# Kernel tuning notes

Hardware: AMD Instinct MI355X
Metric: run time of the kernel (lower is better)

Reference implementation:

```python
import jax, jax.numpy as jnp
import numpy as np

INPUT_DIM = 2048
OUTPUT_DIM = 16000
BATCH = 512


def _make_sketch(key, input_dim, output_dim):
    kh, ks = jax.random.split(key)
    rand_h = jax.random.randint(kh, (input_dim,), 0, output_dim)
    rand_s = (2 * jax.random.randint(ks, (input_dim,), 0, 2) - 1).astype(jnp.float32)
    # count-sketch matrix: one signed nonzero per row (duplicates sum, matching
    # torch.sparse .to_dense())
    return jnp.zeros((input_dim, output_dim), jnp.float32).at[jnp.arange(input_dim), rand_h].add(rand_s)


def setup_inputs() -> dict:
    key = jax.random.key(0)
    k1, k2, k3, k4 = jax.random.split(key, 4)
    return {
        "x1": jax.random.normal(k1, (BATCH, INPUT_DIM), jnp.float32),
        "x2": jax.random.normal(k2, (BATCH, INPUT_DIM), jnp.float32),
        "sketch1": _make_sketch(k3, INPUT_DIM, OUTPUT_DIM),
        "sketch2": _make_sketch(k4, INPUT_DIM, OUTPUT_DIM),
    }


def reference(x1, x2, sketch1, sketch2):
    d = sketch1.shape[1]  # output_dim
    # count-sketch projection (dense GEMM, as in the original)
    p1 = x1 @ sketch1  # [B, D]
    p2 = x2 @ sketch2  # [B, D]
    # circular convolution via FFT
    f1 = jnp.fft.rfft(p1, axis=-1)
    f2 = jnp.fft.rfft(p2, axis=-1)
    # torch.irfft (old API) did NOT normalize -> equals numpy irfft * D; the
    # module then multiplies by output_dim again, matching `* self.output_dim`.
    cbp = jnp.fft.irfft(f1 * f2, n=d, axis=-1) * d
    # signed square root
    ss = jnp.sqrt(jax.nn.relu(cbp)) - jnp.sqrt(jax.nn.relu(-cbp))
    # L2 normalize along dim=0 (the batch dim, as written in the original)
    norm = jnp.sqrt(jnp.sum(ss * ss, axis=0, keepdims=True))
    return ss / jnp.maximum(norm, 1e-12)
```

## Files before the change

### kernel.cpp

```cpp
#include <hip/hip_runtime.h>
#include <math.h>

#define D_OUT 16000
#define IN_DIM 2048
#define BATCH 512
#define T2 1024
#define PAD 129

typedef float floatx4 __attribute__((ext_vector_type(4)));

__device__ __forceinline__ float2 cmul(float2 a, float2 b) {
    return make_float2(a.x * b.x - a.y * b.y, a.x * b.y + a.y * b.x);
}
__device__ __forceinline__ float2 cadd(float2 a, float2 b) { return make_float2(a.x + b.x, a.y + b.y); }
__device__ __forceinline__ float2 csub(float2 a, float2 b) { return make_float2(a.x - b.x, a.y - b.y); }

__device__ __forceinline__ int PZ(int j, int i) { return j * PAD + i; }

template<int INV>
__device__ __forceinline__ float2 ctw(float2 w) { if (INV) w.y = -w.y; return w; }

__device__ __forceinline__ int div125(int m) { return (int)(((unsigned)m * 33555u) >> 22); }

template<int INV>
__device__ __forceinline__ float2 bigtw(int m, const float2* w128f, const float2* wNf) {
    int a = div125(m);
    int b = m - a * 125;
    float2 r = cmul(w128f[a], wNf[b]);
    if (INV) r.y = -r.y;
    return r;
}

template<int INV>
__device__ __forceinline__ void dft5(float2& b0, float2& b1, float2& b2, float2& b3, float2& b4) {
    const float C1 = 0.30901699437494742f, S1 = 0.95105651629515357f;
    const float C2 = -0.80901699437494745f, S2 = 0.58778525229247314f;
    float2 t1 = cadd(b1, b4), t2 = csub(b1, b4);
    float2 t3 = cadd(b2, b3), t4 = csub(b2, b3);
    float2 X0 = make_float2(b0.x + t1.x + t3.x, b0.y + t1.y + t3.y);
    float2 m1 = make_float2(b0.x + C1 * t1.x + C2 * t3.x, b0.y + C1 * t1.y + C2 * t3.y);
    float2 m2 = make_float2(b0.x + C2 * t1.x + C1 * t3.x, b0.y + C2 * t1.y + C1 * t3.y);
    float2 n1 = make_float2(S1 * t2.x + S2 * t4.x, S1 * t2.y + S2 * t4.y);
    float2 n2 = make_float2(S2 * t2.x - S1 * t4.x, S2 * t2.y - S1 * t4.y);
    if (!INV) {
        b1 = make_float2(m1.x + n1.y, m1.y - n1.x);
        b4 = make_float2(m1.x - n1.y, m1.y + n1.x);
        b2 = make_float2(m2.x + n2.y, m2.y - n2.x);
        b3 = make_float2(m2.x - n2.y, m2.y + n2.x);
    } else {
        b1 = make_float2(m1.x - n1.y, m1.y + n1.x);
        b4 = make_float2(m1.x + n1.y, m1.y - n1.x);
        b2 = make_float2(m2.x - n2.y, m2.y + n2.x);
        b3 = make_float2(m2.x + n2.y, m2.y - n2.x);
    }
    b0 = X0;
}

__global__ void extract_kernel(const float* __restrict__ sk1, const float* __restrict__ sk2,
                               int* __restrict__ h1, float* __restrict__ s1,
                               int* __restrict__ h2, float* __restrict__ s2) {
    int row = blockIdx.x & (IN_DIM - 1);
    bool second = blockIdx.x >= IN_DIM;
    const float* sk = second ? sk2 : sk1;
    const floatx4* base = (const floatx4*)(sk + (size_t)row * D_OUT);
    const int t = threadIdx.x;
    float hacc = 0.f, sacc = 0.f;
    floatx4 v[5];
#pragma unroll
    for (int batch = 0; batch < 3; batch++) {
#pragma unroll
        for (int c = 0; c < 5; c++)
            v[c] = __builtin_nontemporal_load(&base[t + 256 * (5 * batch + c)]);
#pragma unroll
        for (int c = 0; c < 5; c++) {
            float j4 = (float)(4 * (t + 256 * (5 * batch + c)));
            hacc += j4 * fabsf(v[c].x) + (j4 + 1.f) * fabsf(v[c].y) +
                    (j4 + 2.f) * fabsf(v[c].z) + (j4 + 3.f) * fabsf(v[c].w);
            sacc += v[c].x + v[c].y + v[c].z + v[c].w;
        }
    }
    if (t < 160) {
        floatx4 vt = __builtin_nontemporal_load(&base[3840 + t]);
        float j4 = (float)(4 * (3840 + t));
        hacc += j4 * fabsf(vt.x) + (j4 + 1.f) * fabsf(vt.y) +
                (j4 + 2.f) * fabsf(vt.z) + (j4 + 3.f) * fabsf(vt.w);
        sacc += vt.x + vt.y + vt.z + vt.w;
    }
#pragma unroll
    for (int off = 32; off; off >>= 1) {
        hacc += __shfl_down(hacc, off);
        sacc += __shfl_down(sacc, off);
    }
    __shared__ float sh[8];
    int lane = t & 63, wv = t >> 6;
    if (lane == 0) { sh[wv] = hacc; sh[wv + 4] = sacc; }
    __syncthreads();
    if (t == 0) {
        float h = sh[0] + sh[1] + sh[2] + sh[3];
        float s = sh[4] + sh[5] + sh[6] + sh[7];
        int* hh = second ? h2 : h1;
        float* ss = second ? s2 : s1;
        hh[row] = (int)(h + 0.5f);
        ss[row] = s;
    }
}

__global__ void __launch_bounds__(T2, 1) cbp_kernel(
    const float* __restrict__ x1, const float* __restrict__ x2,
    const int* __restrict__ h1, const float* __restrict__ s1,
    const int* __restrict__ h2, const float* __restrict__ s2,
    float* __restrict__ out) {
    __shared__ float2 smem[125 * PAD + 1 + 125 + 128 + 125];
    float2* z = smem;
    float2* w125 = smem + 125 * PAD + 1;
    float2* w128f = w125 + 125;
    float2* wNf = w128f + 128;
    const int tid = threadIdx.x;
    const int b = blockIdx.x;

    for (int t = tid; t < 125; t += T2) {
        float s, c;
        sincospif(t * (2.0f / 125.0f), &s, &c);
        w125[t] = make_float2(c, -s);
        sincospif(t * (1.0f / 8000.0f), &s, &c);
        wNf[t] = make_float2(c, -s);
    }
    for (int a = tid; a < 128; a += T2) {
        float s, c;
        sincospif(a * (1.0f / 64.0f), &s, &c);
        w128f[a] = make_float2(c, -s);
    }
    {
        float4* z4 = (float4*)z;
        for (int i = tid; i < 8063; i += T2) z4[i] = make_float4(0.f, 0.f, 0.f, 0.f);
    }
    __syncthreads();

    const float* x1r = x1 + (size_t)b * IN_DIM;
    const float* x2r = x2 + (size_t)b * IN_DIM;
    float* zf = (float*)z;
    for (int i = tid; i < IN_DIM; i += T2) {
        int n1 = h1[i] >> 7, n2 = h1[i] & 127;
        int jr = 25 * (n1 % 5) + 5 * ((n1 / 5) % 5) + n1 / 25;
        atomicAdd(&zf[2 * PZ(jr, n2)], x1r[i] * s1[i]);
        n1 = h2[i] >> 7; n2 = h2[i] & 127;
        jr = 25 * (n1 % 5) + 5 * ((n1 / 5) % 5) + n1 / 25;
        atomicAdd(&zf[2 * PZ(jr, n2) + 1], x2r[i] * s2[i]);
    }
    __syncthreads();

    for (int w = tid; w < 3200; w += T2) {
        int i = w & 127, g = w >> 7;
        int p = PZ(5 * g, i);
        float2 b0 = z[p], b1 = z[p + PAD], b2 = z[p + 2 * PAD], b3 = z[p + 3 * PAD], b4 = z[p + 4 * PAD];
        dft5<0>(b0, b1, b2, b3, b4);
        z[p] = b0; z[p + PAD] = b1; z[p + 2 * PAD] = b2; z[p + 3 * PAD] = b3; z[p + 4 * PAD] = b4;
    }
    __syncthreads();
    for (int w = tid; w < 3200; w += T2) {
        int i = w & 127, j5 = w >> 7;
        int g = j5 / 5, q = j5 - 5 * g;
        int p = PZ(g * 25 + q, i);
        float2 b0 = z[p];
        float2 b1 = cmul(z[p + 5 * PAD], w125[q * 5]);
        float2 b2 = cmul(z[p + 10 * PAD], w125[q * 10]);
        float2 b3 = cmul(z[p + 15 * PAD], w125[q * 15]);
        float2 b4 = cmul(z[p + 20 * PAD], w125[q * 20]);
        dft5<0>(b0, b1, b2, b3, b4);
        z[p] = b0; z[p + 5 * PAD] = b1; z[p + 10 * PAD] = b2; z[p + 15 * PAD] = b3; z[p + 20 * PAD] = b4;
    }
    __syncthreads();
    for (int w = tid; w < 3200; w += T2) {
        int i = w & 127, q = w >> 7;
        int p = PZ(q, i);
        float2 b0 = z[p];
        float2 b1 = cmul(z[p + 25 * PAD], w125[q]);
        float2 b2 = cmul(z[p + 50 * PAD], w125[q * 2]);
        float2 b3 = cmul(z[p + 75 * PAD], w125[q * 3]);
        float2 b4 = cmul(z[p + 100 * PAD], w125[q * 4]);
        dft5<0>(b0, b1, b2, b3, b4);
        z[p]             = cmul(b0, bigtw<0>(i * q, w128f, wNf));
        z[p + 25 * PAD]  = cmul(b1, bigtw<0>(i * (q + 25), w128f, wNf));
        z[p + 50 * PAD]  = cmul(b2, bigtw<0>(i * (q + 50), w128f, wNf));
        z[p + 75 * PAD]  = cmul(b3, bigtw<0>(i * (q + 75), w128f, wNf));
        z[p + 100 * PAD] = cmul(b4, bigtw<0>(i * (q + 100), w128f, wNf));
    }
    __syncthreads();

    if (tid < 1000) {
        int q = tid / 125, j = tid - q * 125;
        int p = PZ(j, q);
        float2 x[16];
#pragma unroll
        for (int t = 0; t < 16; t++) x[t] = z[p + 8 * t];
#pragma unroll
        for (int t = 0; t < 8; t++) {
            float2 u = cadd(x[t], x[t + 8]);
            float2 d = csub(x[t], x[t + 8]);
            x[t + 8] = cmul(d, w128f[q + 8 * t]);
            x[t] = u;
        }
#pragma unroll
        for (int h = 0; h < 16; h += 8)
            for (int t = h; t < h + 4; t++) {
                float2 u = cadd(x[t], x[t + 4]);
                float2 d = csub(x[t], x[t + 4]);
                x[t + 4] = cmul(d, w128f[2 * q + 16 * (t & 7)]);
                x[t] = u;
            }
#pragma unroll
        for (int h = 0; h < 16; h += 4)
            for (int t = h; t < h + 2; t++) {
                float2 u = cadd(x[t], x[t + 2]);
                float2 d = csub(x[t], x[t + 2]);
                x[t + 2] = cmul(d, w128f[4 * q + 32 * (t & 3)]);
                x[t] = u;
            }
        {
            float2 w16 = w128f[8 * q];
#pragma unroll
            for (int t = 0; t < 16; t += 2) {
                float2 u = cadd(x[t], x[t + 1]);
                float2 d = csub(x[t], x[t + 1]);
                x[t + 1] = cmul(d, w16);
                x[t] = u;
            }
        }
#pragma unroll
        for (int t = 0; t < 16; t++) z[p + 8 * t] = x[t];
    }
    __syncthreads();
    for (int idx = tid; idx < 2000; idx += T2) {
        int g = idx / 125, j = idx - g * 125;
        int p = PZ(j, 8 * g);
        float2 x[8];
#pragma unroll
        for (int d = 0; d < 8; d++) x[d] = z[p + d];
#pragma unroll
        for (int d = 0; d < 4; d++) {
            float2 u = cadd(x[d], x[d + 4]);
            float2 v = csub(x[d], x[d + 4]);
            x[d + 4] = cmul(v, w128f[16 * d]);
            x[d] = u;
        }
#pragma unroll
        for (int h = 0; h < 8; h += 4) {
            float2 u = cadd(x[h], x[h + 2]);
            float2 v = csub(x[h], x[h + 2]);
            x[h] = u; x[h + 2] = v;
            u = cadd(x[h + 1], x[h + 3]);
            v = csub(x[h + 1], x[h + 3]);
            x[h + 1] = u;
            x[h + 3] = make_float2(v.y, -v.x);
        }
#pragma unroll
        for (int d = 0; d < 8; d += 2) {
            float2 u = cadd(x[d], x[d + 1]);
            float2 v = csub(x[d], x[d + 1]);
            x[d] = u; x[d + 1] = v;
        }
#pragma unroll
        for (int d = 0; d < 8; d++) z[p + d] = x[d];
    }
    __syncthreads();

    for (int k = tid; k <= 8000; k += T2) {
        int k1 = k % 125, k2 = k / 125;
        int km = (k == 0) ? 0 : 16000 - k;
        int k1m = km % 125, k2m = km / 125;
        int p = PZ(k1, __brev((unsigned)k2) >> 25);
        int pm = PZ(k1m, __brev((unsigned)k2m) >> 25);
        float2 Zk = z[p], Zm = z[pm];
        float2 F1 = make_float2(0.5f * (Zk.x + Zm.x), 0.5f * (Zk.y - Zm.y));
        float2 F2 = make_float2(0.5f * (Zk.y + Zm.y), -0.5f * (Zk.x - Zm.x));
        float2 G = cmul(F1, F2);
        z[p] = G;
        z[pm] = make_float2(G.x, -G.y);
    }
    __syncthreads();

    for (int idx = tid; idx < 2000; idx += T2) {
        int g = idx / 125, j = idx - g * 125;
        int p = PZ(j, 8 * g);
        float2 x[8];
#pragma unroll
        for (int d = 0; d < 8; d++) x[d] = z[p + d];
#pragma unroll
        for (int d = 0; d < 8; d += 2) {
            float2 t = x[d + 1];
            x[d + 1] = csub(x[d], t);
            x[d] = cadd(x[d], t);
        }
#pragma unroll
        for (int h = 0; h < 8; h += 4) {
            float2 t = x[h + 2];
            x[h + 2] = csub(x[h], t);
            x[h] = cadd(x[h], t);
            float2 s = x[h + 3];
            t = make_float2(-s.y, s.x);
            x[h + 3] = csub(x[h + 1], t);
            x[h + 1] = cadd(x[h + 1], t);
        }
#pragma unroll
        for (int d = 0; d < 4; d++) {
            float2 t = cmul(ctw<1>(w128f[16 * d]), x[d + 4]);
            x[d + 4] = csub(x[d], t);
            x[d] = cadd(x[d], t);
        }
#pragma unroll
        for (int d = 0; d < 8; d++) z[p + d] = x[d];
    }
    __syncthreads();
    if (tid < 1000) {
        int q = tid / 125, j = tid - q * 125;
        int p = PZ(j, q);
        float2 x[16];
#pragma unroll
        for (int t = 0; t < 16; t++) x[t] = z[p + 8 * t];
        {
            float2 w16 = ctw<1>(w128f[8 * q]);
#pragma unroll
            for (int t = 0; t < 16; t += 2) {
                float2 tt = cmul(w16, x[t + 1]);
                x[t + 1] = csub(x[t], tt);
                x[t] = cadd(x[t], tt);
            }
        }
#pragma unroll
        for (int h = 0; h < 16; h += 4)
            for (int t = h; t < h + 2; t++) {
                float2 w = ctw<1>(w128f[4 * q + 32 * (t & 3)]);
                float2 tt = cmul(w, x[t + 2]);
                x[t + 2] = csub(x[t], tt);
                x[t] = cadd(x[t], tt);
            }
#pragma unroll
        for (int h = 0; h < 16; h += 8)
            for (int t = h; t < h + 4; t++) {
                float2 w = ctw<1>(w128f[2 * q + 16 * (t & 7)]);
                float2 tt = cmul(w, x[t + 4]);
                x[t + 4] = csub(x[t], tt);
                x[t] = cadd(x[t], tt);
            }
#pragma unroll
        for (int t = 0; t < 8; t++) {
            float2 w = ctw<1>(w128f[q + 8 * t]);
            float2 tt = cmul(w, x[t + 8]);
            x[t + 8] = csub(x[t], tt);
            x[t] = cadd(x[t], tt);
        }
#pragma unroll
        for (int t = 0; t < 16; t++)
            z[p + 8 * t] = cmul(x[t], bigtw<1>((q + 8 * t) * j, w128f, wNf));
    }
    __syncthreads();

    for (int w = tid; w < 3200; w += T2) {
        int i = w & 127, q = w >> 7;
        int p = PZ(q, i);
        float2 b0 = z[p], b1 = z[p + 25 * PAD], b2 = z[p + 50 * PAD],
               b3 = z[p + 75 * PAD], b4 = z[p + 100 * PAD];
        dft5<1>(b0, b1, b2, b3, b4);
        z[p]             = b0;
        z[p + 25 * PAD]  = cmul(b1, ctw<1>(w125[q]));
        z[p + 50 * PAD]  = cmul(b2, ctw<1>(w125[2 * q]));
        z[p + 75 * PAD]  = cmul(b3, ctw<1>(w125[3 * q]));
        z[p + 100 * PAD] = cmul(b4, ctw<1>(w125[4 * q]));
    }
    __syncthreads();
    for (int w = tid; w < 3200; w += T2) {
        int i = w & 127, j5 = w >> 7;
        int u1 = j5 / 5, q2 = j5 - 5 * u1;
        int p = PZ(25 * u1 + q2, i);
        float2 b0 = z[p], b1 = z[p + 5 * PAD], b2 = z[p + 10 * PAD],
               b3 = z[p + 15 * PAD], b4 = z[p + 20 * PAD];
        dft5<1>(b0, b1, b2, b3, b4);
        z[p]            = b0;
        z[p + 5 * PAD]  = cmul(b1, ctw<1>(w125[5 * q2]));
        z[p + 10 * PAD] = cmul(b2, ctw<1>(w125[10 * q2]));
        z[p + 15 * PAD] = cmul(b3, ctw<1>(w125[15 * q2]));
        z[p + 20 * PAD] = cmul(b4, ctw<1>(w125[20 * q2]));
    }
    __syncthreads();
    float* orow = out + (size_t)b * D_OUT;
    for (int w = tid; w < 3200; w += T2) {
        int i = w & 127, g = w >> 7;
        int p = PZ(5 * g, i);
        float2 b0 = z[p], b1 = z[p + PAD], b2 = z[p + 2 * PAD],
               b3 = z[p + 3 * PAD], b4 = z[p + 4 * PAD];
        dft5<1>(b0, b1, b2, b3, b4);
        int g5 = g % 5, gd = g / 5;
        float re[5] = { b0.x, b1.x, b2.x, b3.x, b4.x };
#pragma unroll
        for (int u = 0; u < 5; u++) {
            int n1 = 25 * u + 5 * g5 + gd;
            float c = re[u];
            orow[n1 * 128 + i] = (c > 0.f) ? sqrtf(c) : -sqrtf(-c);
        }
    }
}

__global__ void colsum_kernel(const float* __restrict__ out, float* __restrict__ colsum) {
    __shared__ float sm[512];
    int c = threadIdx.x & 63, r = threadIdx.x >> 6;
    int col = blockIdx.x * 64 + c;
    float acc = 0.f;
    for (int row = r; row < BATCH; row += 8) {
        float v = out[(size_t)row * D_OUT + col];
        acc += v * v;
    }
    sm[threadIdx.x] = acc;
    __syncthreads();
    if (r == 0) {
        float s = sm[c] + sm[c + 64] + sm[c + 128] + sm[c + 192] +
                  sm[c + 256] + sm[c + 320] + sm[c + 384] + sm[c + 448];
        colsum[col] = s;
    }
}

__global__ void normalize_kernel(float* __restrict__ out, const float* __restrict__ colsum) {
    int idx = blockIdx.x * 256 + threadIdx.x;
    float4* o4 = (float4*)out;
    float4 v = o4[idx];
    int n = (idx * 4) % D_OUT;
    const float4 cs = *(const float4*)(colsum + n);
    v.x /= fmaxf(sqrtf(cs.x), 1e-12f);
    v.y /= fmaxf(sqrtf(cs.y), 1e-12f);
    v.z /= fmaxf(sqrtf(cs.z), 1e-12f);
    v.w /= fmaxf(sqrtf(cs.w), 1e-12f);
    o4[idx] = v;
}

extern "C" void kernel_launch(void* const* d_in, const int* in_sizes, int n_in,
                              void* d_out, int out_size, void* d_ws, size_t ws_size,
                              hipStream_t stream) {
    (void)in_sizes; (void)n_in; (void)out_size; (void)ws_size;
    const float* x1 = (const float*)d_in[0];
    const float* x2 = (const float*)d_in[1];
    const float* sk1 = (const float*)d_in[2];
    const float* sk2 = (const float*)d_in[3];
    float* out = (float*)d_out;

    char* ws = (char*)d_ws;
    int* h1 = (int*)(ws);
    float* s1 = (float*)(ws + 8192);
    int* h2 = (int*)(ws + 16384);
    float* s2 = (float*)(ws + 24576);
    float* colsum = (float*)(ws + 32768);

    extract_kernel<<<2 * IN_DIM, 256, 0, stream>>>(sk1, sk2, h1, s1, h2, s2);
    cbp_kernel<<<BATCH, T2, 0, stream>>>(x1, x2, h1, s1, h2, s2, out);
    colsum_kernel<<<250, 512, 0, stream>>>(out, colsum);
    normalize_kernel<<<8000, 256, 0, stream>>>(out, colsum);
}
```

Measured before the change: 357.6 us.

## Compute inverse real FFT as half-length complex FFT via spectrum packing

Replaces the full 16000-point complex inverse FFT, which keeps only real outputs, with an 8000-point complex inverse FFT. Before the inverse, a twiddled combination packs the Hermitian spectrum so that even and odd real outputs come out as real and imaginary parts. This roughly halves the butterfly and shared-memory work in the inverse stages, and the output is written as float2 pairs. The cost is an extra twiddle table, more complex index math in the pointwise stage, and a larger risk of correctness errors in the packing.

```diff
diff --git a/kernel.cpp b/kernel.cpp
--- a/kernel.cpp
+++ b/kernel.cpp
@@ -14,6 +14,8 @@
 }
 __device__ __forceinline__ float2 cadd(float2 a, float2 b) { return make_float2(a.x + b.x, a.y + b.y); }
 __device__ __forceinline__ float2 csub(float2 a, float2 b) { return make_float2(a.x - b.x, a.y - b.y); }
+__device__ __forceinline__ float2 cconj(float2 a) { return make_float2(a.x, -a.y); }
+__device__ __forceinline__ float2 imul(float2 a) { return make_float2(-a.y, a.x); }
 
 __device__ __forceinline__ int PZ(int j, int i) { return j * PAD + i; }
 
@@ -29,6 +31,13 @@
     float2 r = cmul(w128f[a], wNf[b]);
     if (INV) r.y = -r.y;
     return r;
+}
+
+__device__ __forceinline__ float2 bigtw8000inv(int m, const float2* w128f, const float2* w8000f) {
+    int a = div125(m);
+    int b = m - a * 125;
+    float2 r = cmul(w128f[2 * a], w8000f[b]);
+    return make_float2(r.x, -r.y);
 }
 
 template<int INV>
@@ -105,16 +114,28 @@
     }
 }
 
+__device__ __forceinline__ int posk(int k) {
+    int k1 = k % 125, k2 = k / 125;
+    return PZ(k1, (int)(__brev((unsigned)k2) >> 25));
+}
+
+__device__ __forceinline__ float2 crossG(float2 Zk, float2 Zm) {
+    float2 F1 = make_float2(0.5f * (Zk.x + Zm.x), 0.5f * (Zk.y - Zm.y));
+    float2 F2 = make_float2(0.5f * (Zk.y + Zm.y), -0.5f * (Zk.x - Zm.x));
+    return cmul(F1, F2);
+}
+
 __global__ void __launch_bounds__(T2, 1) cbp_kernel(
     const float* __restrict__ x1, const float* __restrict__ x2,
     const int* __restrict__ h1, const float* __restrict__ s1,
     const int* __restrict__ h2, const float* __restrict__ s2,
     float* __restrict__ out) {
-    __shared__ float2 smem[125 * PAD + 1 + 125 + 128 + 125];
+    __shared__ float2 smem[125 * PAD + 1 + 125 + 128 + 125 + 125];
     float2* z = smem;
     float2* w125 = smem + 125 * PAD + 1;
     float2* w128f = w125 + 125;
     float2* wNf = w128f + 128;
+    float2* w8000f = wNf + 125;
     const int tid = threadIdx.x;
     const int b = blockIdx.x;
 
@@ -124,6 +145,8 @@
         w125[t] = make_float2(c, -s);
         sincospif(t * (1.0f / 8000.0f), &s, &c);
         wNf[t] = make_float2(c, -s);
+        sincospif(t * (1.0f / 4000.0f), &s, &c);
+        w8000f[t] = make_float2(c, -s);
     }
     for (int a = tid; a < 128; a += T2) {
         float s, c;
@@ -264,27 +287,29 @@
     }
     __syncthreads();
 
-    for (int k = tid; k <= 8000; k += T2) {
-        int k1 = k % 125, k2 = k / 125;
-        int km = (k == 0) ? 0 : 16000 - k;
-        int k1m = km % 125, k2m = km / 125;
-        int p = PZ(k1, __brev((unsigned)k2) >> 25);
-        int pm = PZ(k1m, __brev((unsigned)k2m) >> 25);
-        float2 Zk = z[p], Zm = z[pm];
-        float2 F1 = make_float2(0.5f * (Zk.x + Zm.x), 0.5f * (Zk.y - Zm.y));
-        float2 F2 = make_float2(0.5f * (Zk.y + Zm.y), -0.5f * (Zk.x - Zm.x));
-        float2 G = cmul(F1, F2);
-        z[p] = G;
-        z[pm] = make_float2(G.x, -G.y);
-    }
-    __syncthreads();
-
-    for (int idx = tid; idx < 2000; idx += T2) {
-        int g = idx / 125, j = idx - g * 125;
-        int p = PZ(j, 8 * g);
+    for (int k = tid; k <= 4000; k += T2) {
+        float2 Zk  = z[posk(k)];
+        float2 Zkm = z[posk(k == 0 ? 0 : 16000 - k)];
+        float2 Zh  = z[posk(8000 - k)];
+        float2 Zhp = z[posk(8000 + k)];
+        float2 G1 = crossG(Zk, Zkm);
+        float2 G2 = crossG(Zh, Zhp);
+        float2 V  = bigtw<1>(k, w128f, wNf);
+        float2 V2 = make_float2(-V.x, V.y);
+        float2 Gc1 = cconj(G1), Gc2 = cconj(G2);
+        float2 C1 = cadd(cadd(G1, Gc2), cmul(V,  imul(csub(G1, Gc2))));
+        float2 C2 = cadd(cadd(G2, Gc1), cmul(V2, imul(csub(G2, Gc1))));
+        z[posk(k)] = C1;
+        if (k > 0) z[posk(8000 - k)] = C2;
+    }
+    __syncthreads();
+
+    if (tid < 1000) {
+        int g = tid / 125, j = tid - g * 125;
+        int p = PZ(j, 16 * g);
         float2 x[8];
 #pragma unroll
-        for (int d = 0; d < 8; d++) x[d] = z[p + d];
+        for (int d = 0; d < 8; d++) x[d] = z[p + 2 * d];
 #pragma unroll
         for (int d = 0; d < 8; d += 2) {
             float2 t = x[d + 1];
@@ -308,56 +333,47 @@
             x[d] = cadd(x[d], t);
         }
 #pragma unroll
-        for (int d = 0; d < 8; d++) z[p + d] = x[d];
+        for (int d = 0; d < 8; d++) z[p + 2 * d] = x[d];
     }
     __syncthreads();
     if (tid < 1000) {
         int q = tid / 125, j = tid - q * 125;
-        int p = PZ(j, q);
-        float2 x[16];
-#pragma unroll
-        for (int t = 0; t < 16; t++) x[t] = z[p + 8 * t];
+        float2 x[8];
+#pragma unroll
+        for (int t = 0; t < 8; t++) x[t] = z[PZ(j, 16 * t + 2 * q)];
         {
             float2 w16 = ctw<1>(w128f[8 * q]);
 #pragma unroll
-            for (int t = 0; t < 16; t += 2) {
+            for (int t = 0; t < 8; t += 2) {
                 float2 tt = cmul(w16, x[t + 1]);
                 x[t + 1] = csub(x[t], tt);
                 x[t] = cadd(x[t], tt);
             }
         }
 #pragma unroll
-        for (int h = 0; h < 16; h += 4)
+        for (int h = 0; h < 8; h += 4)
             for (int t = h; t < h + 2; t++) {
-                float2 w = ctw<1>(w128f[4 * q + 32 * (t & 3)]);
+                float2 w = ctw<1>(w128f[4 * q + 32 * (t & 1)]);
                 float2 tt = cmul(w, x[t + 2]);
                 x[t + 2] = csub(x[t], tt);
                 x[t] = cadd(x[t], tt);
             }
 #pragma unroll
-        for (int h = 0; h < 16; h += 8)
-            for (int t = h; t < h + 4; t++) {
-                float2 w = ctw<1>(w128f[2 * q + 16 * (t & 7)]);
-                float2 tt = cmul(w, x[t + 4]);
-                x[t + 4] = csub(x[t], tt);
-                x[t] = cadd(x[t], tt);
-            }
-#pragma unroll
-        for (int t = 0; t < 8; t++) {
-            float2 w = ctw<1>(w128f[q + 8 * t]);
-            float2 tt = cmul(w, x[t + 8]);
-            x[t + 8] = csub(x[t], tt);
+        for (int t = 0; t < 4; t++) {
+            float2 w = ctw<1>(w128f[2 * q + 16 * t]);
+            float2 tt = cmul(w, x[t + 4]);
+            x[t + 4] = csub(x[t], tt);
             x[t] = cadd(x[t], tt);
         }
 #pragma unroll
-        for (int t = 0; t < 16; t++)
-            z[p + 8 * t] = cmul(x[t], bigtw<1>((q + 8 * t) * j, w128f, wNf));
-    }
-    __syncthreads();
-
-    for (int w = tid; w < 3200; w += T2) {
-        int i = w & 127, q = w >> 7;
-        int p = PZ(q, i);
+        for (int t = 0; t < 8; t++)
+            z[PZ(j, 16 * t + 2 * q)] = cmul(x[t], bigtw8000inv((q + 8 * t) * j, w128f, w8000f));
+    }
+    __syncthreads();
+
+    for (int w = tid; w < 1600; w += T2) {
+        int i6 = w & 63, q = w >> 6;
+        int p = PZ(q, 2 * i6);
         float2 b0 = z[p], b1 = z[p + 25 * PAD], b2 = z[p + 50 * PAD],
                b3 = z[p + 75 * PAD], b4 = z[p + 100 * PAD];
         dft5<1>(b0, b1, b2, b3, b4);
@@ -368,10 +384,10 @@
         z[p + 100 * PAD] = cmul(b4, ctw<1>(w125[4 * q]));
     }
     __syncthreads();
-    for (int w = tid; w < 3200; w += T2) {
-        int i = w & 127, j5 = w >> 7;
+    for (int w = tid; w < 1600; w += T2) {
+        int i6 = w & 63, j5 = w >> 6;
         int u1 = j5 / 5, q2 = j5 - 5 * u1;
-        int p = PZ(25 * u1 + q2, i);
+        int p = PZ(25 * u1 + q2, 2 * i6);
         float2 b0 = z[p], b1 = z[p + 5 * PAD], b2 = z[p + 10 * PAD],
                b3 = z[p + 15 * PAD], b4 = z[p + 20 * PAD];
         dft5<1>(b0, b1, b2, b3, b4);
@@ -382,20 +398,22 @@
         z[p + 20 * PAD] = cmul(b4, ctw<1>(w125[20 * q2]));
     }
     __syncthreads();
-    float* orow = out + (size_t)b * D_OUT;
-    for (int w = tid; w < 3200; w += T2) {
-        int i = w & 127, g = w >> 7;
-        int p = PZ(5 * g, i);
+    float2* orow2 = (float2*)(out + (size_t)b * D_OUT);
+    for (int w = tid; w < 1600; w += T2) {
+        int i6 = w & 63, g = w >> 6;
+        int p = PZ(5 * g, 2 * i6);
         float2 b0 = z[p], b1 = z[p + PAD], b2 = z[p + 2 * PAD],
                b3 = z[p + 3 * PAD], b4 = z[p + 4 * PAD];
         dft5<1>(b0, b1, b2, b3, b4);
         int g5 = g % 5, gd = g / 5;
-        float re[5] = { b0.x, b1.x, b2.x, b3.x, b4.x };
+        float2 wv[5] = { b0, b1, b2, b3, b4 };
 #pragma unroll
         for (int u = 0; u < 5; u++) {
             int n1 = 25 * u + 5 * g5 + gd;
-            float c = re[u];
-            orow[n1 * 128 + i] = (c > 0.f) ? sqrtf(c) : -sqrtf(-c);
+            float re = wv[u].x, im = wv[u].y;
+            float sr = (re > 0.f) ? sqrtf(re) : -sqrtf(-re);
+            float si = (im > 0.f) ? sqrtf(im) : -sqrtf(-im);
+            orow2[64 * n1 + i6] = make_float2(sr, si);
         }
     }
 }
```

New measurement: 348.1 us. -2.7%, faster.
